# Kernel optimization log

Measured on AMD Instinct MI355X. Metric: run time of the kernel, lower is better.

Reference implementation:

```python
import math
import jax, jax.numpy as jnp
import numpy as np

FACTOR = 2  # init kwarg `factor`

def setup_inputs() -> dict:
    key = jax.random.key(0)
    k1, k2, k3 = jax.random.split(key, 3)
    B, H, L, E = 32, 8, 2048, 64
    Q = jax.random.normal(k1, (B, H, L, E), dtype=jnp.float32)
    K = jax.random.normal(k2, (B, H, L, E), dtype=jnp.float32)
    V = jax.random.normal(k3, (B, H, L, E), dtype=jnp.float32)
    return {"Q": Q, "K": K, "V": V}

def _autocorrelation(Q, K, V):
    # Q, K, V: [B, H, L, E]; S == L so the pad/truncate branch is a no-op.
    B, H, L, E = Q.shape
    # FFT-based cross-correlation along the time axis (dim=2)
    q_fft = jnp.fft.rfft(Q, axis=2)
    k_fft = jnp.fft.rfft(K, axis=2)
    corr = jnp.fft.irfft(q_fft * jnp.conj(k_fft), n=L, axis=2)  # [B,H,L,E]
    # time_delay_agg
    top_k = int(FACTOR * math.log(L))  # = 15 for L=2048
    # torch.topk over dim=2 per (b,h,e): move L to last axis for lax.top_k
    weights, delays = jax.lax.top_k(jnp.swapaxes(corr, 2, 3), top_k)  # [B,H,E,k]
    weights = jax.nn.softmax(weights, axis=-1)
    # V.repeat(1,1,2,1) + gather(init+delay) is equivalent to a circular
    # gather from V with index (l + delay) mod L, since 0 <= init+delay <= 2L-2.
    base = jnp.arange(L)  # [L]
    out = jnp.zeros_like(V)
    for i in range(top_k):  # small fixed loop over top_k delays
        d_i = delays[..., i]                       # [B,H,E]
        idx = (base[None, None, :, None] + d_i[:, :, None, :]) % L  # [B,H,L,E]
        pattern = jnp.take_along_axis(V, idx, axis=2)               # [B,H,L,E]
        out = out + pattern * weights[..., i][:, :, None, :]
    return out

def reference(Q, K, V):
    return _autocorrelation(Q, K, V)
```

## Files before the change

kernel.cpp:

```cpp
#include <hip/hip_runtime.h>
#include <math.h>


#define LEN   2048
#define BH    256
#define NE    64
#define NSER  (BH * NE)
#define TOPK  15

__device__ __forceinline__ int IDX(int i) { return i + (i >> 4); }

__device__ __forceinline__ void cmulf(float xr, float xi, float yr, float yi,
                                      float& zr, float& zi) {
  zr = xr * yr - xi * yi;
  zi = xr * yi + xi * yr;
}

__device__ __forceinline__ void sincos_tw(int idx, float& c, float& s) {
  float ang = (float)idx * (-6.283185307179586f / 2048.0f);
  __sincosf(ang, &s, &c);
}

template <bool INV>
__device__ __forceinline__ void dft8(float* xr, float* xi) {
  const float sg = INV ? -1.f : 1.f;
  const float c = 0.70710678118654752440f;
  float s0r = xr[0] + xr[4], s0i = xi[0] + xi[4];
  float s1r = xr[0] - xr[4], s1i = xi[0] - xi[4];
  float s2r = xr[2] + xr[6], s2i = xi[2] + xi[6];
  float s3r = xr[2] - xr[6], s3i = xi[2] - xi[6];
  float E0r = s0r + s2r, E0i = s0i + s2i;
  float E2r = s0r - s2r, E2i = s0i - s2i;
  float E1r = s1r + sg * s3i, E1i = s1i - sg * s3r;
  float E3r = s1r - sg * s3i, E3i = s1i + sg * s3r;
  float u0r = xr[1] + xr[5], u0i = xi[1] + xi[5];
  float u1r = xr[1] - xr[5], u1i = xi[1] - xi[5];
  float u2r = xr[3] + xr[7], u2i = xi[3] + xi[7];
  float u3r = xr[3] - xr[7], u3i = xi[3] - xi[7];
  float O0r = u0r + u2r, O0i = u0i + u2i;
  float O2r = u0r - u2r, O2i = u0i - u2i;
  float O1r = u1r + sg * u3i, O1i = u1i - sg * u3r;
  float O3r = u1r - sg * u3i, O3i = u1i + sg * u3r;
  float G0r = O0r, G0i = O0i;
  float G1r, G1i; cmulf(O1r, O1i, c, -sg * c, G1r, G1i);
  float G2r = sg * O2i, G2i = -sg * O2r;
  float G3r, G3i; cmulf(O3r, O3i, -c, -sg * c, G3r, G3i);
  xr[0] = E0r + G0r; xi[0] = E0i + G0i;
  xr[1] = E1r + G1r; xi[1] = E1i + G1i;
  xr[2] = E2r + G2r; xi[2] = E2i + G2i;
  xr[3] = E3r + G3r; xi[3] = E3i + G3i;
  xr[4] = E0r - G0r; xi[4] = E0i - G0i;
  xr[5] = E1r - G1r; xi[5] = E1i - G1i;
  xr[6] = E2r - G2r; xi[6] = E2i - G2i;
  xr[7] = E3r - G3r; xi[7] = E3i - G3i;
}

template <bool INV>
__device__ __forceinline__ void dft4(float* xr, float* xi) {
  const float sg = INV ? -1.f : 1.f;
  float s0r = xr[0] + xr[2], s0i = xi[0] + xi[2];
  float s1r = xr[0] - xr[2], s1i = xi[0] - xi[2];
  float s2r = xr[1] + xr[3], s2i = xi[1] + xi[3];
  float s3r = xr[1] - xr[3], s3i = xi[1] - xi[3];
  xr[0] = s0r + s2r;        xi[0] = s0i + s2i;
  xr[1] = s1r + sg * s3i;   xi[1] = s1i - sg * s3r;
  xr[2] = s0r - s2r;        xi[2] = s0i - s2i;
  xr[3] = s1r - sg * s3i;   xi[3] = s1i + sg * s3r;
}

template <bool INV>
__device__ __forceinline__ void stage8_mid(const float* inr, const float* ini,
                                           float* outr, float* outi,
                                           int s, int sLog, int t) {
  float ar[8], ai[8];
#pragma unroll
  for (int r = 0; r < 8; ++r) {
    int a = t + 256 * r;
    ar[r] = inr[IDX(a)]; ai[r] = ini[IDX(a)];
  }
  dft8<INV>(ar, ai);
  int q = t & (s - 1), p = t >> sLog;
  int ob = q + 8 * s * p;
  int tb = s * p;
#pragma unroll
  for (int j = 0; j < 8; ++j) {
    float c_, s_;
    sincos_tw(tb * j, c_, s_);
    if (INV) s_ = -s_;
    float zr, zi; cmulf(ar[j], ai[j], c_, s_, zr, zi);
    int o = ob + s * j;
    outr[IDX(o)] = zr; outi[IDX(o)] = zi;
  }
}


__global__ __launch_bounds__(256) void ktrans_qk(const float* __restrict__ Q,
                                                 const float* __restrict__ K,
                                                 float2* __restrict__ ZT) {
  int bh = blockIdx.x >> 5, lt = blockIdx.x & 31, l0 = lt * 64;
  __shared__ float sq[64][65], sk[64][65];
  int col = threadIdx.x & 63, r4 = threadIdx.x >> 6;
  const float* Qb = Q + ((size_t)bh * LEN + l0) * NE;
  const float* Kb = K + ((size_t)bh * LEN + l0) * NE;
#pragma unroll
  for (int it = 0; it < 16; ++it) {
    int row = it * 4 + r4;
    sq[row][col] = Qb[row * NE + col];
    sk[row][col] = Kb[row * NE + col];
  }
  __syncthreads();
  float2* Zb = ZT + (size_t)bh * NE * LEN + l0;
#pragma unroll
  for (int it = 0; it < 16; ++it) {
    int e = it * 4 + r4;
    float2 z; z.x = sq[col][e]; z.y = sk[col][e];
    Zb[(size_t)e * LEN + col] = z;
  }
}

__global__ __launch_bounds__(256) void ktrans_v(const float* __restrict__ src,
                                                float* __restrict__ dst) {
  int bh = blockIdx.x >> 5, lt = blockIdx.x & 31, l0 = lt * 64;
  __shared__ float sT[64][65];
  int col = threadIdx.x & 63, r4 = threadIdx.x >> 6;
  const float* Sb = src + ((size_t)bh * LEN + l0) * NE;
#pragma unroll
  for (int it = 0; it < 16; ++it) {
    int row = it * 4 + r4;
    sT[row][col] = Sb[row * NE + col];
  }
  __syncthreads();
  float* Db = dst + (size_t)bh * NE * LEN + l0;
#pragma unroll
  for (int it = 0; it < 16; ++it) {
    int e = it * 4 + r4;
    Db[(size_t)e * LEN + col] = sT[col][e];
  }
}

__global__ __launch_bounds__(256) void ktrans_o(const float* __restrict__ OT,
                                                float* __restrict__ out) {
  int bh = blockIdx.x >> 5, lt = blockIdx.x & 31, l0 = lt * 64;
  __shared__ float sT[64][65];
  int col = threadIdx.x & 63, r4 = threadIdx.x >> 6;
  const float* Sb = OT + (size_t)bh * NE * LEN + l0;
#pragma unroll
  for (int it = 0; it < 16; ++it) {
    int e = it * 4 + r4;
    sT[e][col] = Sb[(size_t)e * LEN + col];
  }
  __syncthreads();
  float* Ob = out + ((size_t)bh * LEN + l0) * NE;
#pragma unroll
  for (int it = 0; it < 16; ++it) {
    int row = it * 4 + r4;
    Ob[row * NE + col] = sT[col][row];
  }
}


__global__ __launch_bounds__(256) void kfft(const float2* __restrict__ ZT,
                                            float* __restrict__ Wt,
                                            int* __restrict__ Dl) {
  __shared__ float Ar_[2176], Ai_[2176], Br_[2176], Bi_[2176];
  __shared__ float topv[16]; __shared__ int topd[16];
  __shared__ float redv[4]; __shared__ int redi[4];
  const int t = threadIdx.x;
  const int series = blockIdx.x;
  const float2* z = ZT + (size_t)series * LEN;

  {
    float ar[8], ai[8];
#pragma unroll
    for (int r = 0; r < 8; ++r) {
      float2 v = z[t + 256 * r];
      ar[r] = v.x; ai[r] = v.y;
    }
    dft8<false>(ar, ai);
#pragma unroll
    for (int j = 0; j < 8; ++j) {
      float c_, s_;
      sincos_tw(t * j, c_, s_);
      float zr, zi; cmulf(ar[j], ai[j], c_, s_, zr, zi);
      int o = 8 * t + j;
      Ar_[IDX(o)] = zr; Ai_[IDX(o)] = zi;
    }
  }
  __syncthreads();
  stage8_mid<false>(Ar_, Ai_, Br_, Bi_, 8, 3, t);
  __syncthreads();
  stage8_mid<false>(Br_, Bi_, Ar_, Ai_, 64, 6, t);
  __syncthreads();
  {
#pragma unroll
    for (int h = 0; h < 2; ++h) {
      int u = t + 256 * h;
      float xr[4], xi[4];
#pragma unroll
      for (int r = 0; r < 4; ++r) {
        int a = u + 512 * r;
        xr[r] = Ar_[IDX(a)]; xi[r] = Ai_[IDX(a)];
      }
      dft4<false>(xr, xi);
#pragma unroll
      for (int j = 0; j < 4; ++j) {
        int o = u + 512 * j;
        Br_[IDX(o)] = xr[j]; Bi_[IDX(o)] = xi[j];
      }
    }
  }
  __syncthreads();

#pragma unroll
  for (int r = 0; r < 8; ++r) {
    int f = t + 256 * r;
    int m = (LEN - f) & (LEN - 1);
    float zfr = Br_[IDX(f)], zfi = Bi_[IDX(f)];
    float zmr = Br_[IDX(m)], zmi = Bi_[IDX(m)];
    float Xr = 0.5f * (zfr + zmr), Xi = 0.5f * (zfi - zmi);
    float Yr = 0.5f * (zfi + zmi), Yi = -0.5f * (zfr - zmr);
    float Cr = Xr * Yr + Xi * Yi;
    float Ci = Xi * Yr - Xr * Yi;
    Ar_[IDX(f)] = Cr; Ai_[IDX(f)] = Ci;
  }
  __syncthreads();

  stage8_mid<true>(Ar_, Ai_, Br_, Bi_, 1, 0, t);
  __syncthreads();
  stage8_mid<true>(Br_, Bi_, Ar_, Ai_, 8, 3, t);
  __syncthreads();
  stage8_mid<true>(Ar_, Ai_, Br_, Bi_, 64, 6, t);
  __syncthreads();
  float rv[8]; int rix[8];
#pragma unroll
  for (int h = 0; h < 2; ++h) {
    int u = t + 256 * h;
    float xr[4], xi[4];
#pragma unroll
    for (int r = 0; r < 4; ++r) {
      int a = u + 512 * r;
      xr[r] = Br_[IDX(a)]; xi[r] = Bi_[IDX(a)];
    }
    dft4<true>(xr, xi);
#pragma unroll
    for (int j = 0; j < 4; ++j) {
      rv[h * 4 + j] = xr[j];
      rix[h * 4 + j] = u + 512 * j;
    }
  }

  for (int it = 0; it < TOPK; ++it) {
    float bv = rv[0]; int bi_ = rix[0];
#pragma unroll
    for (int k = 1; k < 8; ++k) {
      bool btr = (rv[k] > bv) || (rv[k] == bv && rix[k] < bi_);
      if (btr) { bv = rv[k]; bi_ = rix[k]; }
    }
#pragma unroll
    for (int off = 32; off >= 1; off >>= 1) {
      float ov = __shfl_xor(bv, off);
      int oi = __shfl_xor(bi_, off);
      bool btr = (ov > bv) || (ov == bv && oi < bi_);
      if (btr) { bv = ov; bi_ = oi; }
    }
    if ((t & 63) == 0) { redv[t >> 6] = bv; redi[t >> 6] = bi_; }
    __syncthreads();
    if (t == 0) {
#pragma unroll
      for (int wv = 1; wv < 4; ++wv) {
        bool btr = (redv[wv] > bv) || (redv[wv] == bv && redi[wv] < bi_);
        if (btr) { bv = redv[wv]; bi_ = redi[wv]; }
      }
      topv[it] = bv; topd[it] = bi_;
    }
    __syncthreads();
    int widx = topd[it];
#pragma unroll
    for (int k = 0; k < 8; ++k)
      if (rix[k] == widx) rv[k] = -INFINITY;
  }

  if (t < TOPK) {
    const float scl = 1.0f / 2048.0f;
    float vmax = topv[0];
    float ssum = 0.f;
#pragma unroll
    for (int i = 0; i < TOPK; ++i) ssum += expf((topv[i] - vmax) * scl);
    float wgt = expf((topv[t] - vmax) * scl) / ssum;
    Wt[(size_t)series * 16 + t] = wgt;
    Dl[(size_t)series * 16 + t] = topd[t];
  }
}


__global__ __launch_bounds__(256) void kgather(const float* __restrict__ VT,
                                               const float* __restrict__ Wt,
                                               const int* __restrict__ Dl,
                                               float* __restrict__ OT) {
  __shared__ float v[LEN];
  const int t = threadIdx.x;
  const int series = blockIdx.x;
  const float4* src = (const float4*)(VT + (size_t)series * LEN);
  float4* vv = (float4*)v;
#pragma unroll
  for (int i = 0; i < 2; ++i) vv[t + 256 * i] = src[t + 256 * i];
  float w[TOPK]; int d[TOPK];
#pragma unroll
  for (int i = 0; i < TOPK; ++i) {
    w[i] = Wt[(size_t)series * 16 + i];
    d[i] = Dl[(size_t)series * 16 + i];
  }
  __syncthreads();
  float* dst = OT + (size_t)series * LEN;
#pragma unroll
  for (int r = 0; r < 8; ++r) {
    int l = t + 256 * r;
    float acc = 0.f;
#pragma unroll
    for (int i = 0; i < TOPK; ++i) acc += w[i] * v[(l + d[i]) & (LEN - 1)];
    dst[l] = acc;
  }
}

extern "C" void kernel_launch(void* const* d_in, const int* in_sizes, int n_in,
                              void* d_out, int out_size, void* d_ws, size_t ws_size,
                              hipStream_t stream) {
  const float* Q = (const float*)d_in[0];
  const float* K = (const float*)d_in[1];
  const float* V = (const float*)d_in[2];
  float* out = (float*)d_out;
  char* ws = (char*)d_ws;

  const size_t ZT_BYTES = (size_t)NSER * LEN * sizeof(float2);
  float2* ZT = (float2*)ws;
  float* Wt = (float*)(ws + ZT_BYTES);
  int* Dl = (int*)(ws + ZT_BYTES + (size_t)NSER * 16 * sizeof(float));
  float* OT = (float*)ws;
  float* VT = out;

  ktrans_qk<<<BH * 32, 256, 0, stream>>>(Q, K, ZT);
  kfft<<<NSER, 256, 0, stream>>>(ZT, Wt, Dl);
  ktrans_v<<<BH * 32, 256, 0, stream>>>(V, VT);
  kgather<<<NSER, 256, 0, stream>>>(VT, Wt, Dl, OT);
  ktrans_o<<<BH * 32, 256, 0, stream>>>(OT, out);
}
```

Measured before the change: 894.8 us.

## Vectorize transposes, halve FFT LDS with in-place stages, per-wave top-k merge

The three transpose kernels now use float4 global loads and stores in place of scalar accesses. The FFT kernel drops the ping-pong buffers and runs every radix stage in place on one Re/Im pair, which roughly halves shared memory and lets launch_bounds ask for 8 blocks per CU. The conjugate-symmetric spectrum product is now computed once per f/m pair. Top-k selection keeps a separate candidate list per wave with no block barriers inside the loop, then merges the four lists in one wave using shuffles. The cost is extra barriers inside each in-place stage and a second merge pass.

Measured after the change: 885.7 us. No clear change (-1.0%).

```diff
diff --git a/kernel.cpp b/kernel.cpp
--- a/kernel.cpp
+++ b/kernel.cpp
@@ -7,6 +7,7 @@
 #define NE    64
 #define NSER  (BH * NE)
 #define TOPK  15
+#define NINF  (-INFINITY)
 
 __device__ __forceinline__ int IDX(int i) { return i + (i >> 4); }
 
@@ -69,15 +70,15 @@
 }
 
 template <bool INV>
-__device__ __forceinline__ void stage8_mid(const float* inr, const float* ini,
-                                           float* outr, float* outi,
-                                           int s, int sLog, int t) {
+__device__ __forceinline__ void stage8_ip(float* Re, float* Im,
+                                          int s, int sLog, int t) {
   float ar[8], ai[8];
 #pragma unroll
   for (int r = 0; r < 8; ++r) {
     int a = t + 256 * r;
-    ar[r] = inr[IDX(a)]; ai[r] = ini[IDX(a)];
-  }
+    ar[r] = Re[IDX(a)]; ai[r] = Im[IDX(a)];
+  }
+  __syncthreads();
   dft8<INV>(ar, ai);
   int q = t & (s - 1), p = t >> sLog;
   int ob = q + 8 * s * p;
@@ -89,85 +90,107 @@
     if (INV) s_ = -s_;
     float zr, zi; cmulf(ar[j], ai[j], c_, s_, zr, zi);
     int o = ob + s * j;
-    outr[IDX(o)] = zr; outi[IDX(o)] = zi;
-  }
+    Re[IDX(o)] = zr; Im[IDX(o)] = zi;
+  }
+  __syncthreads();
 }
 
 
 __global__ __launch_bounds__(256) void ktrans_qk(const float* __restrict__ Q,
                                                  const float* __restrict__ K,
                                                  float2* __restrict__ ZT) {
-  int bh = blockIdx.x >> 5, lt = blockIdx.x & 31, l0 = lt * 64;
+  int bh = blockIdx.x >> 5, l0 = (blockIdx.x & 31) * 64;
   __shared__ float sq[64][65], sk[64][65];
-  int col = threadIdx.x & 63, r4 = threadIdx.x >> 6;
-  const float* Qb = Q + ((size_t)bh * LEN + l0) * NE;
-  const float* Kb = K + ((size_t)bh * LEN + l0) * NE;
-#pragma unroll
-  for (int it = 0; it < 16; ++it) {
-    int row = it * 4 + r4;
-    sq[row][col] = Qb[row * NE + col];
-    sk[row][col] = Kb[row * NE + col];
+  int t = threadIdx.x;
+  const float4* Qb = (const float4*)(Q + ((size_t)bh * LEN + l0) * NE);
+  const float4* Kb = (const float4*)(K + ((size_t)bh * LEN + l0) * NE);
+  int x = t & 15, c4 = x * 4;
+#pragma unroll
+  for (int it = 0; it < 4; ++it) {
+    int row = (t >> 4) + it * 16;
+    float4 q4 = Qb[row * 16 + x];
+    float4 k4 = Kb[row * 16 + x];
+    sq[row][c4 + 0] = q4.x; sq[row][c4 + 1] = q4.y;
+    sq[row][c4 + 2] = q4.z; sq[row][c4 + 3] = q4.w;
+    sk[row][c4 + 0] = k4.x; sk[row][c4 + 1] = k4.y;
+    sk[row][c4 + 2] = k4.z; sk[row][c4 + 3] = k4.w;
   }
   __syncthreads();
   float2* Zb = ZT + (size_t)bh * NE * LEN + l0;
-#pragma unroll
-  for (int it = 0; it < 16; ++it) {
-    int e = it * 4 + r4;
-    float2 z; z.x = sq[col][e]; z.y = sk[col][e];
-    Zb[(size_t)e * LEN + col] = z;
+  int l2 = (t & 31) * 2;
+#pragma unroll
+  for (int it = 0; it < 8; ++it) {
+    int e = (t >> 5) + it * 8;
+    float4 o;
+    o.x = sq[l2][e];     o.y = sk[l2][e];
+    o.z = sq[l2 + 1][e]; o.w = sk[l2 + 1][e];
+    *(float4*)&Zb[(size_t)e * LEN + l2] = o;
   }
 }
 
 __global__ __launch_bounds__(256) void ktrans_v(const float* __restrict__ src,
                                                 float* __restrict__ dst) {
-  int bh = blockIdx.x >> 5, lt = blockIdx.x & 31, l0 = lt * 64;
+  int bh = blockIdx.x >> 5, l0 = (blockIdx.x & 31) * 64;
   __shared__ float sT[64][65];
-  int col = threadIdx.x & 63, r4 = threadIdx.x >> 6;
-  const float* Sb = src + ((size_t)bh * LEN + l0) * NE;
-#pragma unroll
-  for (int it = 0; it < 16; ++it) {
-    int row = it * 4 + r4;
-    sT[row][col] = Sb[row * NE + col];
+  int t = threadIdx.x;
+  const float4* Sb = (const float4*)(src + ((size_t)bh * LEN + l0) * NE);
+  int x = t & 15, c4 = x * 4;
+#pragma unroll
+  for (int it = 0; it < 4; ++it) {
+    int row = (t >> 4) + it * 16;
+    float4 v4 = Sb[row * 16 + x];
+    sT[row][c4 + 0] = v4.x; sT[row][c4 + 1] = v4.y;
+    sT[row][c4 + 2] = v4.z; sT[row][c4 + 3] = v4.w;
   }
   __syncthreads();
   float* Db = dst + (size_t)bh * NE * LEN + l0;
-#pragma unroll
-  for (int it = 0; it < 16; ++it) {
-    int e = it * 4 + r4;
-    Db[(size_t)e * LEN + col] = sT[col][e];
+  int l4 = x * 4;
+#pragma unroll
+  for (int it = 0; it < 4; ++it) {
+    int e = (t >> 4) + it * 16;
+    float4 o;
+    o.x = sT[l4 + 0][e]; o.y = sT[l4 + 1][e];
+    o.z = sT[l4 + 2][e]; o.w = sT[l4 + 3][e];
+    *(float4*)&Db[(size_t)e * LEN + l4] = o;
   }
 }
 
 __global__ __launch_bounds__(256) void ktrans_o(const float* __restrict__ OT,
                                                 float* __restrict__ out) {
-  int bh = blockIdx.x >> 5, lt = blockIdx.x & 31, l0 = lt * 64;
+  int bh = blockIdx.x >> 5, l0 = (blockIdx.x & 31) * 64;
   __shared__ float sT[64][65];
-  int col = threadIdx.x & 63, r4 = threadIdx.x >> 6;
+  int t = threadIdx.x;
   const float* Sb = OT + (size_t)bh * NE * LEN + l0;
-#pragma unroll
-  for (int it = 0; it < 16; ++it) {
-    int e = it * 4 + r4;
-    sT[e][col] = Sb[(size_t)e * LEN + col];
+  int x = t & 15, l4 = x * 4;
+#pragma unroll
+  for (int it = 0; it < 4; ++it) {
+    int e = (t >> 4) + it * 16;
+    float4 v4 = *(const float4*)&Sb[(size_t)e * LEN + l4];
+    sT[e][l4 + 0] = v4.x; sT[e][l4 + 1] = v4.y;
+    sT[e][l4 + 2] = v4.z; sT[e][l4 + 3] = v4.w;
   }
   __syncthreads();
   float* Ob = out + ((size_t)bh * LEN + l0) * NE;
-#pragma unroll
-  for (int it = 0; it < 16; ++it) {
-    int row = it * 4 + r4;
-    Ob[row * NE + col] = sT[col][row];
-  }
-}
-
-
-__global__ __launch_bounds__(256) void kfft(const float2* __restrict__ ZT,
-                                            float* __restrict__ Wt,
-                                            int* __restrict__ Dl) {
-  __shared__ float Ar_[2176], Ai_[2176], Br_[2176], Bi_[2176];
-  __shared__ float topv[16]; __shared__ int topd[16];
-  __shared__ float redv[4]; __shared__ int redi[4];
+  int e4 = x * 4;
+#pragma unroll
+  for (int it = 0; it < 4; ++it) {
+    int row = (t >> 4) + it * 16;
+    float4 o;
+    o.x = sT[e4 + 0][row]; o.y = sT[e4 + 1][row];
+    o.z = sT[e4 + 2][row]; o.w = sT[e4 + 3][row];
+    *(float4*)&Ob[row * NE + e4] = o;
+  }
+}
+
+
+__global__ __launch_bounds__(256, 8) void kfft(const float2* __restrict__ ZT,
+                                               float* __restrict__ Wt,
+                                               int* __restrict__ Dl) {
+  __shared__ float Re[2176], Im[2176];
+  __shared__ float mv[64]; __shared__ int mi[64];
   const int t = threadIdx.x;
-  const int series = blockIdx.x;
-  const float2* z = ZT + (size_t)series * LEN;
+  const int wv = t >> 6, ln = t & 63;
+  const float2* z = ZT + (size_t)blockIdx.x * LEN;
 
   {
     float ar[8], ai[8];
@@ -183,55 +206,12 @@
       sincos_tw(t * j, c_, s_);
       float zr, zi; cmulf(ar[j], ai[j], c_, s_, zr, zi);
       int o = 8 * t + j;
-      Ar_[IDX(o)] = zr; Ai_[IDX(o)] = zi;
-    }
-  }
-  __syncthreads();
-  stage8_mid<false>(Ar_, Ai_, Br_, Bi_, 8, 3, t);
-  __syncthreads();
-  stage8_mid<false>(Br_, Bi_, Ar_, Ai_, 64, 6, t);
-  __syncthreads();
-  {
-#pragma unroll
-    for (int h = 0; h < 2; ++h) {
-      int u = t + 256 * h;
-      float xr[4], xi[4];
-#pragma unroll
-      for (int r = 0; r < 4; ++r) {
-        int a = u + 512 * r;
-        xr[r] = Ar_[IDX(a)]; xi[r] = Ai_[IDX(a)];
-      }
-      dft4<false>(xr, xi);
-#pragma unroll
-      for (int j = 0; j < 4; ++j) {
-        int o = u + 512 * j;
-        Br_[IDX(o)] = xr[j]; Bi_[IDX(o)] = xi[j];
-      }
-    }
-  }
-  __syncthreads();
-
-#pragma unroll
-  for (int r = 0; r < 8; ++r) {
-    int f = t + 256 * r;
-    int m = (LEN - f) & (LEN - 1);
-    float zfr = Br_[IDX(f)], zfi = Bi_[IDX(f)];
-    float zmr = Br_[IDX(m)], zmi = Bi_[IDX(m)];
-    float Xr = 0.5f * (zfr + zmr), Xi = 0.5f * (zfi - zmi);
-    float Yr = 0.5f * (zfi + zmi), Yi = -0.5f * (zfr - zmr);
-    float Cr = Xr * Yr + Xi * Yi;
-    float Ci = Xi * Yr - Xr * Yi;
-    Ar_[IDX(f)] = Cr; Ai_[IDX(f)] = Ci;
-  }
-  __syncthreads();
-
-  stage8_mid<true>(Ar_, Ai_, Br_, Bi_, 1, 0, t);
-  __syncthreads();
-  stage8_mid<true>(Br_, Bi_, Ar_, Ai_, 8, 3, t);
-  __syncthreads();
-  stage8_mid<true>(Ar_, Ai_, Br_, Bi_, 64, 6, t);
-  __syncthreads();
-  float rv[8]; int rix[8];
+      Re[IDX(o)] = zr; Im[IDX(o)] = zi;
+    }
+  }
+  __syncthreads();
+  stage8_ip<false>(Re, Im, 8, 3, t);
+  stage8_ip<false>(Re, Im, 64, 6, t);
 #pragma unroll
   for (int h = 0; h < 2; ++h) {
     int u = t + 256 * h;
@@ -239,56 +219,118 @@
 #pragma unroll
     for (int r = 0; r < 4; ++r) {
       int a = u + 512 * r;
-      xr[r] = Br_[IDX(a)]; xi[r] = Bi_[IDX(a)];
+      xr[r] = Re[IDX(a)]; xi[r] = Im[IDX(a)];
+    }
+    dft4<false>(xr, xi);
+#pragma unroll
+    for (int j = 0; j < 4; ++j) {
+      int o = u + 512 * j;
+      Re[IDX(o)] = xr[j]; Im[IDX(o)] = xi[j];
+    }
+  }
+  __syncthreads();
+
+  {
+    float zfr[4], zfi[4], zmr[4], zmi[4];
+#pragma unroll
+    for (int r = 0; r < 4; ++r) {
+      int f = t + 256 * r;
+      int m = (LEN - f) & (LEN - 1);
+      zfr[r] = Re[IDX(f)]; zfi[r] = Im[IDX(f)];
+      zmr[r] = Re[IDX(m)]; zmi[r] = Im[IDX(m)];
+    }
+    float e1r = 0.f, e1i = 0.f;
+    if (t == 0) { e1r = Re[IDX(1024)]; e1i = Im[IDX(1024)]; }
+    __syncthreads();
+#pragma unroll
+    for (int r = 0; r < 4; ++r) {
+      int f = t + 256 * r;
+      int m = (LEN - f) & (LEN - 1);
+      float Xr = 0.5f * (zfr[r] + zmr[r]), Xi = 0.5f * (zfi[r] - zmi[r]);
+      float Yr = 0.5f * (zfi[r] + zmi[r]), Yi = -0.5f * (zfr[r] - zmr[r]);
+      Re[IDX(f)] = Xr * Yr + Xi * Yi;
+      Im[IDX(f)] = Xi * Yr - Xr * Yi;
+      float Xr2 = 0.5f * (zmr[r] + zfr[r]), Xi2 = 0.5f * (zmi[r] - zfi[r]);
+      float Yr2 = 0.5f * (zfi[r] + zmi[r]), Yi2 = -0.5f * (zmr[r] - zfr[r]);
+      Re[IDX(m)] = Xr2 * Yr2 + Xi2 * Yi2;
+      Im[IDX(m)] = Xi2 * Yr2 - Xr2 * Yi2;
+    }
+    if (t == 0) {
+      Re[IDX(1024)] = e1r * e1i;
+      Im[IDX(1024)] = 0.f;
+    }
+  }
+  __syncthreads();
+
+  stage8_ip<true>(Re, Im, 1, 0, t);
+  stage8_ip<true>(Re, Im, 8, 3, t);
+  stage8_ip<true>(Re, Im, 64, 6, t);
+  float rv[8];
+#pragma unroll
+  for (int h = 0; h < 2; ++h) {
+    int u = t + 256 * h;
+    float xr[4], xi[4];
+#pragma unroll
+    for (int r = 0; r < 4; ++r) {
+      int a = u + 512 * r;
+      xr[r] = Re[IDX(a)]; xi[r] = Im[IDX(a)];
     }
     dft4<true>(xr, xi);
 #pragma unroll
-    for (int j = 0; j < 4; ++j) {
-      rv[h * 4 + j] = xr[j];
-      rix[h * 4 + j] = u + 512 * j;
-    }
+    for (int j = 0; j < 4; ++j) rv[h * 4 + j] = xr[j];
   }
 
   for (int it = 0; it < TOPK; ++it) {
-    float bv = rv[0]; int bi_ = rix[0];
+    float bv = rv[0]; int bidx = t;
 #pragma unroll
     for (int k = 1; k < 8; ++k) {
-      bool btr = (rv[k] > bv) || (rv[k] == bv && rix[k] < bi_);
-      if (btr) { bv = rv[k]; bi_ = rix[k]; }
+      int ik = t + 256 * (k >> 2) + 512 * (k & 3);
+      bool btr = (rv[k] > bv) || (rv[k] == bv && ik < bidx);
+      if (btr) { bv = rv[k]; bidx = ik; }
     }
 #pragma unroll
     for (int off = 32; off >= 1; off >>= 1) {
       float ov = __shfl_xor(bv, off);
-      int oi = __shfl_xor(bi_, off);
-      bool btr = (ov > bv) || (ov == bv && oi < bi_);
-      if (btr) { bv = ov; bi_ = oi; }
-    }
-    if ((t & 63) == 0) { redv[t >> 6] = bv; redi[t >> 6] = bi_; }
-    __syncthreads();
-    if (t == 0) {
-#pragma unroll
-      for (int wv = 1; wv < 4; ++wv) {
-        bool btr = (redv[wv] > bv) || (redv[wv] == bv && redi[wv] < bi_);
-        if (btr) { bv = redv[wv]; bi_ = redi[wv]; }
+      int oi = __shfl_xor(bidx, off);
+      bool btr = (ov > bv) || (ov == bv && oi < bidx);
+      if (btr) { bv = ov; bidx = oi; }
+    }
+    if (ln == 0) { mv[wv * 16 + it] = bv; mi[wv * 16 + it] = bidx; }
+    int d = bidx - t;
+#pragma unroll
+    for (int k = 0; k < 8; ++k) {
+      int ck = 256 * (k >> 2) + 512 * (k & 3);
+      if (d == ck) rv[k] = NINF;
+    }
+  }
+  __syncthreads();
+
+  if (wv == 0) {
+    float v = ((ln & 15) < TOPK) ? mv[ln] : NINF;
+    int ix = ((ln & 15) < TOPK) ? mi[ln] : 0;
+    float myv = NINF; int myi = 0;
+    for (int it = 0; it < TOPK; ++it) {
+      float bv = v; int bidx = ix;
+#pragma unroll
+      for (int off = 32; off >= 1; off >>= 1) {
+        float ov = __shfl_xor(bv, off);
+        int oi = __shfl_xor(bidx, off);
+        bool btr = (ov > bv) || (ov == bv && oi < bidx);
+        if (btr) { bv = ov; bidx = oi; }
       }
-      topv[it] = bv; topd[it] = bi_;
-    }
-    __syncthreads();
-    int widx = topd[it];
-#pragma unroll
-    for (int k = 0; k < 8; ++k)
-      if (rix[k] == widx) rv[k] = -INFINITY;
-  }
-
-  if (t < TOPK) {
+      if (ln == it) { myv = bv; myi = bidx; }
+      if (ix == bidx) v = NINF;
+    }
     const float scl = 1.0f / 2048.0f;
-    float vmax = topv[0];
-    float ssum = 0.f;
-#pragma unroll
-    for (int i = 0; i < TOPK; ++i) ssum += expf((topv[i] - vmax) * scl);
-    float wgt = expf((topv[t] - vmax) * scl) / ssum;
-    Wt[(size_t)series * 16 + t] = wgt;
-    Dl[(size_t)series * 16 + t] = topd[t];
+    float vmax = __shfl(myv, 0);
+    float e = (ln < TOPK) ? expf((myv - vmax) * scl) : 0.f;
+    float ssum = e;
+#pragma unroll
+    for (int off = 1; off < 16; off <<= 1) ssum += __shfl_xor(ssum, off);
+    if (ln < TOPK) {
+      Wt[(size_t)blockIdx.x * 16 + ln] = e / ssum;
+      Dl[(size_t)blockIdx.x * 16 + ln] = myi;
+    }
   }
 }
 
```
